# Optimization experiments

Hardware: AMD Instinct MI355X
Metric: run time of the kernel (lower is better)

## Reference

```python
import jax, jax.numpy as jnp
import numpy as np

NUM_GRAPHS = 512
EPS_BN = 1e-5


def _bn(x, g, b):
    # BatchNorm1d in training mode: biased batch statistics over node dim
    m = x.mean(0)
    v = x.var(0)
    return g * (x - m) * jax.lax.rsqrt(v + EPS_BN) + b


def _gcn(x, W, b, src, dst):
    # GCNConv with self-loops and symmetric deg^-1/2 normalization
    n = x.shape[0]
    loop = jnp.arange(n, dtype=src.dtype)
    s = jnp.concatenate([src, loop])
    d = jnp.concatenate([dst, loop])
    h = x @ W  # [N, C_out]
    deg = jax.ops.segment_sum(jnp.ones(d.shape[0], dtype=h.dtype), d, num_segments=n)
    dinv = jax.lax.rsqrt(jnp.maximum(deg, 1.0))  # deg >= 1 due to self-loops
    norm = dinv[s] * dinv[d]  # [E+N]
    out = jax.ops.segment_sum(norm[:, None] * h[s], d, num_segments=n)
    return out + b


def setup_inputs() -> dict:
    key = jax.random.key(0)
    ks = jax.random.split(key, 16)
    N, E, F = 100000, 1600000, 6

    def lin(k, fi, fo):
        k1, k2 = jax.random.split(k)
        s = 1.0 / np.sqrt(fi)
        return (jax.random.uniform(k1, (fi, fo), minval=-s, maxval=s),
                jax.random.uniform(k2, (fo,), minval=-s, maxval=s))

    W1, b1 = lin(ks[0], F, 32)
    W2, b2 = lin(ks[1], 32, 64)
    W3, b3 = lin(ks[2], 64, 128)
    Wf1, bf1 = lin(ks[3], 128, 128)
    Wf2, bf2 = lin(ks[4], 128, 64)
    return {
        "x": jax.random.normal(ks[5], (N, F), dtype=jnp.float32),
        "edge_src": jax.random.randint(ks[6], (E,), 0, N, dtype=jnp.int32),
        "edge_dst": jax.random.randint(ks[7], (E,), 0, N, dtype=jnp.int32),
        "batch": jnp.sort(jax.random.randint(ks[8], (N,), 0, NUM_GRAPHS, dtype=jnp.int32)),
        "W1": W1, "b1": b1, "g1": jnp.ones(32), "be1": jnp.zeros(32),
        "W2": W2, "b2": b2, "g2": jnp.ones(64), "be2": jnp.zeros(64),
        "W3": W3, "b3": b3, "g3": jnp.ones(128), "be3": jnp.zeros(128),
        "Wf1": Wf1, "bf1": bf1, "g4": jnp.ones(128), "be4": jnp.zeros(128),
        "Wf2": Wf2, "bf2": bf2,
    }


def reference(x, edge_src, edge_dst, batch,
              W1, b1, g1, be1, W2, b2, g2, be2, W3, b3, g3, be3,
              Wf1, bf1, g4, be4, Wf2, bf2):
    h = jax.nn.relu(_bn(_gcn(x, W1, b1, edge_src, edge_dst), g1, be1))
    h = jax.nn.relu(_bn(_gcn(h, W2, b2, edge_src, edge_dst), g2, be2))
    h = jax.nn.relu(_bn(_gcn(h, W3, b3, edge_src, edge_dst), g3, be3))
    p = jax.ops.segment_max(h, batch, num_segments=NUM_GRAPHS)  # [G, 128]
    p = jax.nn.relu(_bn(p @ Wf1 + bf1, g4, be4))  # dropout = identity (eval)
    p = p @ Wf2 + bf2
    return p / jnp.maximum(jnp.linalg.norm(p, axis=1, keepdims=True), 1e-12)
```

## Files before the change

### kernel.cpp

```cpp
#include <hip/hip_runtime.h>
#include <hip/hip_bf16.h>

#define NG 512
#define EPS_BN 1e-5f

__device__ __forceinline__ float4 f4add(float4 a, float4 b) {
    a.x += b.x; a.y += b.y; a.z += b.z; a.w += b.w; return a;
}
__device__ __forceinline__ float4 f4fma(float s, float4 b, float4 a) {
    a.x = fmaf(s, b.x, a.x); a.y = fmaf(s, b.y, a.y);
    a.z = fmaf(s, b.z, a.z); a.w = fmaf(s, b.w, a.w); return a;
}
__device__ __forceinline__ float4 f4scale(float s, float4 a) {
    a.x *= s; a.y *= s; a.z *= s; a.w *= s; return a;
}
__device__ __forceinline__ float4 bnrelu4(float4 v, float4 sc, float4 sh) {
    float4 r;
    r.x = fmaxf(fmaf(sc.x, v.x, sh.x), 0.f);
    r.y = fmaxf(fmaf(sc.y, v.y, sh.y), 0.f);
    r.z = fmaxf(fmaf(sc.z, v.z, sh.z), 0.f);
    r.w = fmaxf(fmaf(sc.w, v.w, sh.w), 0.f);
    return r;
}
__device__ __forceinline__ void bnparam(float sm, float sq, float ga, float bt,
                                        float invN, float& sc, float& sh) {
    float m = sm * invN;
    float var = fmaf(-m, m, sq * invN);
    sc = ga * rsqrtf(var + EPS_BN);
    sh = fmaf(-m, sc, bt);
}


__global__ void k_count(const int* __restrict__ dst, int* __restrict__ cnt, int E) {
    int i = blockIdx.x * blockDim.x + threadIdx.x;
    if (i < E) atomicAdd(&cnt[dst[i]], 1);
}

__global__ void k_dinv(const int* __restrict__ cnt, float* __restrict__ dinv, int N) {
    int i = blockIdx.x * blockDim.x + threadIdx.x;
    if (i < N) dinv[i] = rsqrtf((float)cnt[i] + 1.0f);
}


#define SCAN_T 256
#define SCAN_I 4

__global__ void k_scan1(const int* __restrict__ in, int* __restrict__ out,
                        int* __restrict__ bsum, int N) {
    __shared__ int lds[SCAN_T];
    int t = threadIdx.x;
    int base = blockIdx.x * (SCAN_T * SCAN_I) + t * SCAN_I;
    int v[SCAN_I];
    int sum = 0;
#pragma unroll
    for (int i = 0; i < SCAN_I; ++i) {
        int idx = base + i;
        v[i] = (idx < N) ? in[idx] : 0;
        sum += v[i];
    }
    lds[t] = sum;
    __syncthreads();
    for (int o = 1; o < SCAN_T; o <<= 1) {
        int a = (t >= o) ? lds[t - o] : 0;
        __syncthreads();
        lds[t] += a;
        __syncthreads();
    }
    int run = lds[t] - sum;
#pragma unroll
    for (int i = 0; i < SCAN_I; ++i) {
        int idx = base + i;
        if (idx < N) out[idx] = run;
        run += v[i];
    }
    if (t == SCAN_T - 1) bsum[blockIdx.x] = lds[SCAN_T - 1];
}

__global__ void k_scan2(int* __restrict__ bs, int nb) {
    __shared__ int lds[SCAN_T];
    int t = threadIdx.x;
    int runbase = 0;
    for (int start = 0; start < nb; start += SCAN_T) {
        int idx = start + t;
        int v = (idx < nb) ? bs[idx] : 0;
        lds[t] = v;
        __syncthreads();
        for (int o = 1; o < SCAN_T; o <<= 1) {
            int a = (t >= o) ? lds[t - o] : 0;
            __syncthreads();
            lds[t] += a;
            __syncthreads();
        }
        if (idx < nb) bs[idx] = runbase + lds[t] - v;
        int tot = lds[SCAN_T - 1];
        __syncthreads();
        runbase += tot;
    }
}

__global__ void k_scan3(int* __restrict__ out, const int* __restrict__ bs, int N) {
    int add = bs[blockIdx.x];
    int base = blockIdx.x * (SCAN_T * SCAN_I) + threadIdx.x * SCAN_I;
#pragma unroll
    for (int i = 0; i < SCAN_I; ++i) {
        int idx = base + i;
        if (idx < N) out[idx] += add;
    }
}


__global__ void k_bucket(const int* __restrict__ src, const int* __restrict__ dst,
                         const float* __restrict__ dinv, const int* __restrict__ rowptr,
                         int* __restrict__ fill, int* __restrict__ esrc,
                         float* __restrict__ ewt, int E) {
    int e = blockIdx.x * blockDim.x + threadIdx.x;
    if (e >= E) return;
    int d = dst[e], s = src[e];
    int pos = rowptr[d] + atomicAdd(&fill[d], 1);
    esrc[pos] = s;
    ewt[pos] = dinv[s];
}


template <int COUT>
__global__ __launch_bounds__(256) void k_layer1(
    const int* __restrict__ rowptr, const int* __restrict__ cnt,
    const int* __restrict__ esrc, const float* __restrict__ ewt,
    const float* __restrict__ dinv, const float* __restrict__ x,
    const float* __restrict__ W, float* __restrict__ hout,
    float* __restrict__ sums, float* __restrict__ sumsq, int N) {
    constexpr int NPB = 256;
    constexpr int CG = COUT / 4;
    constexpr int RPB = 256 / CG;
    __shared__ float4 inT4[NPB * 6 / 4];
    float* inT = (float*)inT4;
    __shared__ float4 wT[6 * CG];
    __shared__ float4 red[256];
    int t = threadIdx.x;
    const float4* W4 = (const float4*)W;
    for (int i = t; i < 6 * CG; i += 256) wT[i] = W4[i];
    int base = blockIdx.x * NPB;
    int n = base + t;
    if (n < N) {
        const float2* x2 = (const float2*)x;
        int beg = rowptr[n], end = beg + cnt[n];
        float di = dinv[n];
        size_t b3 = (size_t)n * 3;
        float2 p0 = x2[b3], p1 = x2[b3 + 1], p2 = x2[b3 + 2];
        float a0 = di * p0.x, a1 = di * p0.y, a2 = di * p1.x;
        float a3 = di * p1.y, a4 = di * p2.x, a5 = di * p2.y;
        for (int e = beg; e < end; ++e) {
            int s = esrc[e];
            float w = ewt[e];
            size_t s3 = (size_t)s * 3;
            float2 q0 = x2[s3], q1 = x2[s3 + 1], q2 = x2[s3 + 2];
            a0 = fmaf(w, q0.x, a0); a1 = fmaf(w, q0.y, a1);
            a2 = fmaf(w, q1.x, a2); a3 = fmaf(w, q1.y, a3);
            a4 = fmaf(w, q2.x, a4); a5 = fmaf(w, q2.y, a5);
        }
        int o = t * 6;
        inT[o + 0] = di * a0; inT[o + 1] = di * a1; inT[o + 2] = di * a2;
        inT[o + 3] = di * a3; inT[o + 4] = di * a4; inT[o + 5] = di * a5;
    }
    __syncthreads();
    int gi = t % CG, r0 = t / CG, c0 = gi * 4;
    int nrows = min(NPB, N - base);
    float4 s = {0, 0, 0, 0}, s2 = {0, 0, 0, 0};
    for (int r = r0; r < nrows; r += RPB) {
        const float* row = inT + r * 6;
        float4 acc = {0, 0, 0, 0};
#pragma unroll
        for (int k = 0; k < 6; ++k) acc = f4fma(row[k], wT[k * CG + gi], acc);
        reinterpret_cast<float4*>(hout + (size_t)(base + r) * COUT)[gi] = acc;
        s = f4add(s, acc);
        s2.x = fmaf(acc.x, acc.x, s2.x);
        s2.y = fmaf(acc.y, acc.y, s2.y);
        s2.z = fmaf(acc.z, acc.z, s2.z);
        s2.w = fmaf(acc.w, acc.w, s2.w);
    }
    red[t] = s;
    for (int hh = RPB / 2; hh > 0; hh >>= 1) {
        __syncthreads();
        if (r0 < hh) red[t] = f4add(red[t], red[t + hh * CG]);
    }
    if (r0 == 0) {
        float4 a = red[t];
        atomicAdd(&sums[c0 + 0], a.x); atomicAdd(&sums[c0 + 1], a.y);
        atomicAdd(&sums[c0 + 2], a.z); atomicAdd(&sums[c0 + 3], a.w);
    }
    __syncthreads();
    red[t] = s2;
    for (int hh = RPB / 2; hh > 0; hh >>= 1) {
        __syncthreads();
        if (r0 < hh) red[t] = f4add(red[t], red[t + hh * CG]);
    }
    if (r0 == 0) {
        float4 b = red[t];
        atomicAdd(&sumsq[c0 + 0], b.x); atomicAdd(&sumsq[c0 + 1], b.y);
        atomicAdd(&sumsq[c0 + 2], b.z); atomicAdd(&sumsq[c0 + 3], b.w);
    }
}


template <int CIN, int COUT, int NPB>
__global__ __launch_bounds__(256, 5) void k_layer(
    const int* __restrict__ rowptr, const int* __restrict__ cnt,
    const int* __restrict__ esrc, const float* __restrict__ ewt,
    const float* __restrict__ dinv, const float* __restrict__ hin,
    const float* __restrict__ sums_in, const float* __restrict__ sumsq_in,
    const float* __restrict__ gam, const float* __restrict__ bet,
    const float* __restrict__ W, float* __restrict__ hout,
    float* __restrict__ sums_out, float* __restrict__ sumsq_out,
    int N, float invN) {
    constexpr int TPN = CIN / 4;
    constexpr int PAD = TPN + 1;
    constexpr int ITER1 = NPB * TPN / 256;
    constexpr int NPI = 256 / TPN;
    constexpr int CG = COUT / 4;
    constexpr int RPB = 256 / CG;
    __shared__ float4 inT4[NPB * PAD];
    __shared__ float4 red[256];
    int t = threadIdx.x;
    const float4* W4 = (const float4*)W;
    int base = blockIdx.x * NPB;
    {
        int c4 = t % TPN;
        float4 sm = reinterpret_cast<const float4*>(sums_in)[c4];
        float4 sq = reinterpret_cast<const float4*>(sumsq_in)[c4];
        float4 ga = reinterpret_cast<const float4*>(gam)[c4];
        float4 bt = reinterpret_cast<const float4*>(bet)[c4];
        float4 sc, sh;
        bnparam(sm.x, sq.x, ga.x, bt.x, invN, sc.x, sh.x);
        bnparam(sm.y, sq.y, ga.y, bt.y, invN, sc.y, sh.y);
        bnparam(sm.z, sq.z, ga.z, bt.z, invN, sc.z, sh.z);
        bnparam(sm.w, sq.w, ga.w, bt.w, invN, sc.w, sh.w);
        const float4* h4 = reinterpret_cast<const float4*>(hin);
#pragma unroll
        for (int it = 0; it < ITER1; ++it) {
            int nl = it * NPI + t / TPN;
            int n = base + nl;
            if (n < N) {
                int beg = rowptr[n], end = beg + cnt[n];
                float di = dinv[n];
                float4 acc = f4scale(di, bnrelu4(h4[(size_t)n * TPN + c4], sc, sh));
                int e = beg;
                for (; e + 3 < end; e += 4) {
                    int s0 = esrc[e], s1 = esrc[e + 1], s2_ = esrc[e + 2], s3_ = esrc[e + 3];
                    float w0 = ewt[e], w1 = ewt[e + 1], w2 = ewt[e + 2], w3 = ewt[e + 3];
                    float4 v0 = h4[(size_t)s0 * TPN + c4];
                    float4 v1 = h4[(size_t)s1 * TPN + c4];
                    float4 v2 = h4[(size_t)s2_ * TPN + c4];
                    float4 v3 = h4[(size_t)s3_ * TPN + c4];
                    acc = f4fma(w0, bnrelu4(v0, sc, sh), acc);
                    acc = f4fma(w1, bnrelu4(v1, sc, sh), acc);
                    acc = f4fma(w2, bnrelu4(v2, sc, sh), acc);
                    acc = f4fma(w3, bnrelu4(v3, sc, sh), acc);
                }
                for (; e + 1 < end; e += 2) {
                    int s0 = esrc[e], s1 = esrc[e + 1];
                    float w0 = ewt[e], w1 = ewt[e + 1];
                    float4 v0 = h4[(size_t)s0 * TPN + c4];
                    float4 v1 = h4[(size_t)s1 * TPN + c4];
                    acc = f4fma(w0, bnrelu4(v0, sc, sh), acc);
                    acc = f4fma(w1, bnrelu4(v1, sc, sh), acc);
                }
                if (e < end)
                    acc = f4fma(ewt[e], bnrelu4(h4[(size_t)esrc[e] * TPN + c4], sc, sh), acc);
                inT4[nl * PAD + c4] = f4scale(di, acc);
            }
        }
    }
    __syncthreads();
    int gi = t % CG, r0 = t / CG, c0 = gi * 4;
    int nrows = min(NPB, N - base);
    float4 s = {0, 0, 0, 0}, s2 = {0, 0, 0, 0};
    for (int r = r0; r < nrows; r += RPB) {
        const float* row = (const float*)(inT4 + r * PAD);
        float4 acc = {0, 0, 0, 0};
#pragma unroll 8
        for (int k = 0; k < CIN; ++k) acc = f4fma(row[k], W4[k * CG + gi], acc);
        reinterpret_cast<float4*>(hout + (size_t)(base + r) * COUT)[gi] = acc;
        s = f4add(s, acc);
        s2.x = fmaf(acc.x, acc.x, s2.x);
        s2.y = fmaf(acc.y, acc.y, s2.y);
        s2.z = fmaf(acc.z, acc.z, s2.z);
        s2.w = fmaf(acc.w, acc.w, s2.w);
    }
    red[t] = s;
    for (int hh = RPB / 2; hh > 0; hh >>= 1) {
        __syncthreads();
        if (r0 < hh) red[t] = f4add(red[t], red[t + hh * CG]);
    }
    if (r0 == 0) {
        float4 a = red[t];
        atomicAdd(&sums_out[c0 + 0], a.x); atomicAdd(&sums_out[c0 + 1], a.y);
        atomicAdd(&sums_out[c0 + 2], a.z); atomicAdd(&sums_out[c0 + 3], a.w);
    }
    __syncthreads();
    red[t] = s2;
    for (int hh = RPB / 2; hh > 0; hh >>= 1) {
        __syncthreads();
        if (r0 < hh) red[t] = f4add(red[t], red[t + hh * CG]);
    }
    if (r0 == 0) {
        float4 b = red[t];
        atomicAdd(&sumsq_out[c0 + 0], b.x); atomicAdd(&sumsq_out[c0 + 1], b.y);
        atomicAdd(&sumsq_out[c0 + 2], b.z); atomicAdd(&sumsq_out[c0 + 3], b.w);
    }
}


template <int CIN, int COUT, int ROWS>
__global__ __launch_bounds__(256) void k_mm_stats(
    const float* __restrict__ in, const float* __restrict__ W,
    float* __restrict__ out, float* __restrict__ sums,
    float* __restrict__ sumsq, int N) {
    constexpr int CG = COUT / 4;
    constexpr int RPB = 256 / CG;
    __shared__ float4 inT4[ROWS * CIN / 4];
    float* inT = (float*)inT4;
    __shared__ float4 wT[CIN * CG];
    __shared__ float4 red[256];
    int t = threadIdx.x;
    const float4* W4 = reinterpret_cast<const float4*>(W);
    for (int i = t; i < CIN * CG; i += 256) wT[i] = W4[i];
    int base = blockIdx.x * ROWS;
    int nrows = min(ROWS, N - base);
    {
        const float4* in4 = reinterpret_cast<const float4*>(in + (size_t)base * CIN);
        int tot = nrows * (CIN / 4);
        for (int i = t; i < tot; i += 256) inT4[i] = in4[i];
    }
    __syncthreads();
    int gi = t % CG, r0 = t / CG, c0 = gi * 4;
    float4 s = {0, 0, 0, 0}, s2 = {0, 0, 0, 0};
    for (int r = r0; r < nrows; r += RPB) {
        const float* row = inT + r * CIN;
        float4 acc = {0, 0, 0, 0};
#pragma unroll
        for (int k = 0; k < CIN; ++k) acc = f4fma(row[k], wT[k * CG + gi], acc);
        reinterpret_cast<float4*>(out + (size_t)(base + r) * COUT)[gi] = acc;
        s = f4add(s, acc);
        s2.x = fmaf(acc.x, acc.x, s2.x);
        s2.y = fmaf(acc.y, acc.y, s2.y);
        s2.z = fmaf(acc.z, acc.z, s2.z);
        s2.w = fmaf(acc.w, acc.w, s2.w);
    }
    red[t] = s;
    for (int hh = RPB / 2; hh > 0; hh >>= 1) {
        __syncthreads();
        if (r0 < hh) red[t] = f4add(red[t], red[t + hh * CG]);
    }
    if (r0 == 0) {
        float4 a = red[t];
        atomicAdd(&sums[c0 + 0], a.x); atomicAdd(&sums[c0 + 1], a.y);
        atomicAdd(&sums[c0 + 2], a.z); atomicAdd(&sums[c0 + 3], a.w);
    }
    __syncthreads();
    red[t] = s2;
    for (int hh = RPB / 2; hh > 0; hh >>= 1) {
        __syncthreads();
        if (r0 < hh) red[t] = f4add(red[t], red[t + hh * CG]);
    }
    if (r0 == 0) {
        float4 b = red[t];
        atomicAdd(&sumsq[c0 + 0], b.x); atomicAdd(&sumsq[c0 + 1], b.y);
        atomicAdd(&sumsq[c0 + 2], b.z); atomicAdd(&sumsq[c0 + 3], b.w);
    }
}


__global__ void k_segmax_bn(const float* __restrict__ h, const int* __restrict__ batch,
                            const float* __restrict__ sums, const float* __restrict__ sumsq,
                            const float* __restrict__ gam, const float* __restrict__ bet,
                            float* __restrict__ pool, int N, float invN) {
    int t = threadIdx.x;
    int c = t & 127;
    int sub = t >> 7;
    int base = blockIdx.x * 64 + sub * 32;
    if (base >= N) return;
    float sc, sh;
    bnparam(sums[c], sumsq[c], gam[c], bet[c], invN, sc, sh);
    int cur = batch[base];
    float mx = fmaxf(fmaf(sc, h[(size_t)base * 128 + c], sh), 0.f);
    int lim = min(32, N - base);
    for (int i = 1; i < lim; ++i) {
        int n = base + i;
        int b = batch[n];
        float v = fmaxf(fmaf(sc, h[(size_t)n * 128 + c], sh), 0.f);
        if (b != cur) {
            atomicMax(reinterpret_cast<int*>(pool) + (cur << 7) + c, __float_as_int(mx));
            cur = b; mx = v;
        } else {
            mx = fmaxf(mx, v);
        }
    }
    atomicMax(reinterpret_cast<int*>(pool) + (cur << 7) + c, __float_as_int(mx));
}


__global__ void k_head(const float* __restrict__ Z, const float* __restrict__ sums,
                       const float* __restrict__ sumsq, const float* __restrict__ gam,
                       const float* __restrict__ bet, const float* __restrict__ Wf2,
                       const float* __restrict__ bf2, float* __restrict__ out) {
    int g = blockIdx.x, c = threadIdx.x;
    __shared__ float row[128];
    const float invG = 1.0f / (float)NG;
    for (int j = c; j < 128; j += 64) {
        float sc, sh;
        bnparam(sums[j], sumsq[j], gam[j], bet[j], invG, sc, sh);
        row[j] = fmaxf(fmaf(sc, Z[(g << 7) + j], sh), 0.f);
    }
    __syncthreads();
    float acc = bf2[c];
#pragma unroll
    for (int k = 0; k < 128; ++k) acc = fmaf(row[k], Wf2[k * 64 + c], acc);
    float ss = acc * acc;
#pragma unroll
    for (int off = 32; off; off >>= 1) ss += __shfl_xor(ss, off);
    out[(g << 6) + c] = acc / fmaxf(sqrtf(ss), 1e-12f);
}


extern "C" void kernel_launch(void* const* d_in, const int* in_sizes, int n_in,
                              void* d_out, int out_size, void* d_ws, size_t ws_size,
                              hipStream_t stream) {
    const float* x    = (const float*)d_in[0];
    const int*   src  = (const int*)d_in[1];
    const int*   dst  = (const int*)d_in[2];
    const int*   batch= (const int*)d_in[3];
    const float* W1   = (const float*)d_in[4];
    const float* g1   = (const float*)d_in[6];
    const float* be1  = (const float*)d_in[7];
    const float* W2   = (const float*)d_in[8];
    const float* g2   = (const float*)d_in[10];
    const float* be2  = (const float*)d_in[11];
    const float* W3   = (const float*)d_in[12];
    const float* g3   = (const float*)d_in[14];
    const float* be3  = (const float*)d_in[15];
    const float* Wf1  = (const float*)d_in[16];
    const float* g4   = (const float*)d_in[18];
    const float* be4  = (const float*)d_in[19];
    const float* Wf2  = (const float*)d_in[20];
    const float* bf2  = (const float*)d_in[21];
    float* out = (float*)d_out;

    const int N = in_sizes[0] / 6;
    const int E = in_sizes[1];
    const int nScanBlocks = (N + SCAN_T * SCAN_I - 1) / (SCAN_T * SCAN_I);

    char* ws = (char*)d_ws;
    size_t off = 0;
    auto carve = [&](size_t bytes) {
        void* p = ws + off;
        off += (bytes + 255) & ~(size_t)255;
        return p;
    };
    int*   cnt    = (int*)carve((size_t)N * 4);
    float* dinv   = (float*)carve((size_t)N * 4);
    int*   rowptr = (int*)carve((size_t)N * 4);
    int*   fill   = (int*)carve((size_t)N * 4);
    int*   bsum   = (int*)carve((size_t)4096 * 4);
    int*   esrc   = (int*)carve((size_t)E * 4);
    float* ewt    = (float*)carve((size_t)E * 4);
    float* H1     = (float*)carve((size_t)N * 32 * 4);
    float* H2     = (float*)carve((size_t)N * 64 * 4);
    float* H3     = (float*)carve((size_t)N * 128 * 4);
    float* stats  = (float*)carve(704 * 4);
    float* pool   = (float*)carve((size_t)NG * 128 * 4);
    float* Z      = (float*)carve((size_t)NG * 128 * 4);
    float* s1 = stats;
    float* s2 = stats + 64;
    float* s3 = stats + 192;
    float* s4 = stats + 448;

    const float invN = 1.0f / (float)N;

    hipMemsetAsync(cnt, 0, (size_t)N * 4, stream);
    hipMemsetAsync(fill, 0, (size_t)N * 4, stream);
    hipMemsetAsync(stats, 0, 704 * 4, stream);
    hipMemsetAsync(pool, 0, (size_t)NG * 128 * 4, stream);
    k_count<<<(E + 255) / 256, 256, 0, stream>>>(dst, cnt, E);
    k_dinv<<<(N + 255) / 256, 256, 0, stream>>>(cnt, dinv, N);
    k_scan1<<<nScanBlocks, SCAN_T, 0, stream>>>(cnt, rowptr, bsum, N);
    k_scan2<<<1, SCAN_T, 0, stream>>>(bsum, nScanBlocks);
    k_scan3<<<nScanBlocks, SCAN_T, 0, stream>>>(rowptr, bsum, N);
    k_bucket<<<(E + 255) / 256, 256, 0, stream>>>(src, dst, dinv, rowptr, fill, esrc, ewt, E);

    k_layer1<32><<<(N + 255) / 256, 256, 0, stream>>>(
        rowptr, cnt, esrc, ewt, dinv, x, W1, H1, s1, s1 + 32, N);

    k_layer<32, 64, 64><<<(N + 63) / 64, 256, 0, stream>>>(
        rowptr, cnt, esrc, ewt, dinv, H1, s1, s1 + 32, g1, be1, W2, H2,
        s2, s2 + 64, N, invN);

    k_layer<64, 128, 64><<<(N + 63) / 64, 256, 0, stream>>>(
        rowptr, cnt, esrc, ewt, dinv, H2, s2, s2 + 64, g2, be2, W3, H3,
        s3, s3 + 128, N, invN);

    k_segmax_bn<<<(N + 63) / 64, 256, 0, stream>>>(H3, batch, s3, s3 + 128, g3, be3, pool, N, invN);

    k_mm_stats<128, 128, 64><<<(NG + 63) / 64, 256, 0, stream>>>(pool, Wf1, Z, s4, s4 + 128, NG);
    k_head<<<NG, 64, 0, stream>>>(Z, s4, s4 + 128, g4, be4, Wf2, bf2, out);
}
```

Baseline: 815.1 us.

## Split each node's edge list across lanes and pack edge src/weight pairs

Packs each CSR edge's source index and weight into one int2 array, so the aggregation loops do one 8-byte load per edge instead of two separate loads. Layer 1 and the hidden-layer kernels now split each node's neighbour list across 4 lanes and combine the partial sums with xor shuffles. This raises memory-level parallelism in the gather loops and spreads work more evenly across nodes of different degree. Blocks now process 32 nodes (NPB 32) with a higher occupancy launch bound, at the cost of more blocks and extra shuffle traffic.

```diff
diff --git a/kernel.cpp b/kernel.cpp
--- a/kernel.cpp
+++ b/kernel.cpp
@@ -28,6 +28,13 @@
     float var = fmaf(-m, m, sq * invN);
     sc = ga * rsqrtf(var + EPS_BN);
     sh = fmaf(-m, sc, bt);
+}
+__device__ __forceinline__ float4 f4shflxor_add(float4 a, int m) {
+    a.x += __shfl_xor(a.x, m);
+    a.y += __shfl_xor(a.y, m);
+    a.z += __shfl_xor(a.z, m);
+    a.w += __shfl_xor(a.w, m);
+    return a;
 }
 
 
@@ -111,56 +118,87 @@
 
 __global__ void k_bucket(const int* __restrict__ src, const int* __restrict__ dst,
                          const float* __restrict__ dinv, const int* __restrict__ rowptr,
-                         int* __restrict__ fill, int* __restrict__ esrc,
-                         float* __restrict__ ewt, int E) {
+                         int* __restrict__ fill, int2* __restrict__ e2, int E) {
     int e = blockIdx.x * blockDim.x + threadIdx.x;
     if (e >= E) return;
     int d = dst[e], s = src[e];
     int pos = rowptr[d] + atomicAdd(&fill[d], 1);
-    esrc[pos] = s;
-    ewt[pos] = dinv[s];
+    e2[pos] = make_int2(s, __float_as_int(dinv[s]));
 }
 
 
 template <int COUT>
 __global__ __launch_bounds__(256) void k_layer1(
     const int* __restrict__ rowptr, const int* __restrict__ cnt,
-    const int* __restrict__ esrc, const float* __restrict__ ewt,
-    const float* __restrict__ dinv, const float* __restrict__ x,
-    const float* __restrict__ W, float* __restrict__ hout,
-    float* __restrict__ sums, float* __restrict__ sumsq, int N) {
+    const int2* __restrict__ e2, const float* __restrict__ dinv,
+    const float* __restrict__ x, const float* __restrict__ W,
+    float* __restrict__ hout, float* __restrict__ sums,
+    float* __restrict__ sumsq, int N) {
     constexpr int NPB = 256;
     constexpr int CG = COUT / 4;
     constexpr int RPB = 256 / CG;
-    __shared__ float4 inT4[NPB * 6 / 4];
-    float* inT = (float*)inT4;
+    __shared__ float inT[NPB * 6];
     __shared__ float4 wT[6 * CG];
     __shared__ float4 red[256];
     int t = threadIdx.x;
     const float4* W4 = (const float4*)W;
     for (int i = t; i < 6 * CG; i += 256) wT[i] = W4[i];
     int base = blockIdx.x * NPB;
-    int n = base + t;
-    if (n < N) {
+    {
         const float2* x2 = (const float2*)x;
-        int beg = rowptr[n], end = beg + cnt[n];
-        float di = dinv[n];
-        size_t b3 = (size_t)n * 3;
-        float2 p0 = x2[b3], p1 = x2[b3 + 1], p2 = x2[b3 + 2];
-        float a0 = di * p0.x, a1 = di * p0.y, a2 = di * p1.x;
-        float a3 = di * p1.y, a4 = di * p2.x, a5 = di * p2.y;
-        for (int e = beg; e < end; ++e) {
-            int s = esrc[e];
-            float w = ewt[e];
-            size_t s3 = (size_t)s * 3;
-            float2 q0 = x2[s3], q1 = x2[s3 + 1], q2 = x2[s3 + 2];
-            a0 = fmaf(w, q0.x, a0); a1 = fmaf(w, q0.y, a1);
-            a2 = fmaf(w, q1.x, a2); a3 = fmaf(w, q1.y, a3);
-            a4 = fmaf(w, q2.x, a4); a5 = fmaf(w, q2.y, a5);
+        int ew = t & 3;
+        int nl0 = t >> 2;
+#pragma unroll 1
+        for (int it = 0; it < 4; ++it) {
+            int nl = it * 64 + nl0;
+            int n = base + nl;
+            float a0 = 0, a1 = 0, a2 = 0, a3 = 0, a4 = 0, a5 = 0;
+            float di = 0.f;
+            if (n < N) {
+                di = dinv[n];
+                int beg = rowptr[n], end = beg + cnt[n];
+                if (ew == 0) {
+                    size_t b3 = (size_t)n * 3;
+                    float2 p0 = x2[b3], p1 = x2[b3 + 1], p2 = x2[b3 + 2];
+                    a0 = di * p0.x; a1 = di * p0.y; a2 = di * p1.x;
+                    a3 = di * p1.y; a4 = di * p2.x; a5 = di * p2.y;
+                }
+                int e = beg + ew;
+                for (; e + 4 < end; e += 8) {
+                    int2 pa = e2[e], pb = e2[e + 4];
+                    size_t sa = (size_t)pa.x * 3, sb = (size_t)pb.x * 3;
+                    float2 qa0 = x2[sa], qa1 = x2[sa + 1], qa2 = x2[sa + 2];
+                    float2 qb0 = x2[sb], qb1 = x2[sb + 1], qb2 = x2[sb + 2];
+                    float wa = __int_as_float(pa.y), wb = __int_as_float(pb.y);
+                    a0 = fmaf(wa, qa0.x, a0); a1 = fmaf(wa, qa0.y, a1);
+                    a2 = fmaf(wa, qa1.x, a2); a3 = fmaf(wa, qa1.y, a3);
+                    a4 = fmaf(wa, qa2.x, a4); a5 = fmaf(wa, qa2.y, a5);
+                    a0 = fmaf(wb, qb0.x, a0); a1 = fmaf(wb, qb0.y, a1);
+                    a2 = fmaf(wb, qb1.x, a2); a3 = fmaf(wb, qb1.y, a3);
+                    a4 = fmaf(wb, qb2.x, a4); a5 = fmaf(wb, qb2.y, a5);
+                }
+                if (e < end) {
+                    int2 pa = e2[e];
+                    size_t sa = (size_t)pa.x * 3;
+                    float2 qa0 = x2[sa], qa1 = x2[sa + 1], qa2 = x2[sa + 2];
+                    float wa = __int_as_float(pa.y);
+                    a0 = fmaf(wa, qa0.x, a0); a1 = fmaf(wa, qa0.y, a1);
+                    a2 = fmaf(wa, qa1.x, a2); a3 = fmaf(wa, qa1.y, a3);
+                    a4 = fmaf(wa, qa2.x, a4); a5 = fmaf(wa, qa2.y, a5);
+                }
+            }
+#pragma unroll
+            for (int m = 1; m < 4; m <<= 1) {
+                a0 += __shfl_xor(a0, m); a1 += __shfl_xor(a1, m);
+                a2 += __shfl_xor(a2, m); a3 += __shfl_xor(a3, m);
+                a4 += __shfl_xor(a4, m); a5 += __shfl_xor(a5, m);
+            }
+            if (ew == 0 && n < N) {
+                int o = nl * 6;
+                inT[o + 0] = di * a0; inT[o + 1] = di * a1; inT[o + 2] = di * a2;
+                inT[o + 3] = di * a3; inT[o + 4] = di * a4; inT[o + 5] = di * a5;
+            }
         }
-        int o = t * 6;
-        inT[o + 0] = di * a0; inT[o + 1] = di * a1; inT[o + 2] = di * a2;
-        inT[o + 3] = di * a3; inT[o + 4] = di * a4; inT[o + 5] = di * a5;
     }
     __syncthreads();
     int gi = t % CG, r0 = t / CG, c0 = gi * 4;
@@ -202,20 +240,21 @@
 }
 
 
-template <int CIN, int COUT, int NPB>
-__global__ __launch_bounds__(256, 5) void k_layer(
+template <int CIN, int COUT, int NPB, int EW>
+__global__ __launch_bounds__(256, 8) void k_layer(
     const int* __restrict__ rowptr, const int* __restrict__ cnt,
-    const int* __restrict__ esrc, const float* __restrict__ ewt,
-    const float* __restrict__ dinv, const float* __restrict__ hin,
+    const int2* __restrict__ e2, const float* __restrict__ dinv,
+    const float* __restrict__ hin,
     const float* __restrict__ sums_in, const float* __restrict__ sumsq_in,
     const float* __restrict__ gam, const float* __restrict__ bet,
     const float* __restrict__ W, float* __restrict__ hout,
     float* __restrict__ sums_out, float* __restrict__ sumsq_out,
     int N, float invN) {
     constexpr int TPN = CIN / 4;
+    constexpr int LPN = TPN * EW;
+    constexpr int NPI = 256 / LPN;
+    constexpr int ITER1 = NPB / NPI;
     constexpr int PAD = TPN + 1;
-    constexpr int ITER1 = NPB * TPN / 256;
-    constexpr int NPI = 256 / TPN;
     constexpr int CG = COUT / 4;
     constexpr int RPB = 256 / CG;
     __shared__ float4 inT4[NPB * PAD];
@@ -225,6 +264,8 @@
     int base = blockIdx.x * NPB;
     {
         int c4 = t % TPN;
+        int ew = (t % LPN) / TPN;
+        int nl0 = t / LPN;
         float4 sm = reinterpret_cast<const float4*>(sums_in)[c4];
         float4 sq = reinterpret_cast<const float4*>(sumsq_in)[c4];
         float4 ga = reinterpret_cast<const float4*>(gam)[c4];
@@ -235,39 +276,34 @@
         bnparam(sm.z, sq.z, ga.z, bt.z, invN, sc.z, sh.z);
         bnparam(sm.w, sq.w, ga.w, bt.w, invN, sc.w, sh.w);
         const float4* h4 = reinterpret_cast<const float4*>(hin);
-#pragma unroll
+#pragma unroll 1
         for (int it = 0; it < ITER1; ++it) {
-            int nl = it * NPI + t / TPN;
+            int nl = it * NPI + nl0;
             int n = base + nl;
+            float4 acc = {0, 0, 0, 0};
+            float di = 0.f;
             if (n < N) {
+                di = dinv[n];
                 int beg = rowptr[n], end = beg + cnt[n];
-                float di = dinv[n];
-                float4 acc = f4scale(di, bnrelu4(h4[(size_t)n * TPN + c4], sc, sh));
-                int e = beg;
-                for (; e + 3 < end; e += 4) {
-                    int s0 = esrc[e], s1 = esrc[e + 1], s2_ = esrc[e + 2], s3_ = esrc[e + 3];
-                    float w0 = ewt[e], w1 = ewt[e + 1], w2 = ewt[e + 2], w3 = ewt[e + 3];
-                    float4 v0 = h4[(size_t)s0 * TPN + c4];
-                    float4 v1 = h4[(size_t)s1 * TPN + c4];
-                    float4 v2 = h4[(size_t)s2_ * TPN + c4];
-                    float4 v3 = h4[(size_t)s3_ * TPN + c4];
-                    acc = f4fma(w0, bnrelu4(v0, sc, sh), acc);
-                    acc = f4fma(w1, bnrelu4(v1, sc, sh), acc);
-                    acc = f4fma(w2, bnrelu4(v2, sc, sh), acc);
-                    acc = f4fma(w3, bnrelu4(v3, sc, sh), acc);
+                if (ew == 0)
+                    acc = f4scale(di, bnrelu4(h4[(size_t)n * TPN + c4], sc, sh));
+                int e = beg + ew;
+                for (; e + EW < end; e += 2 * EW) {
+                    int2 pa = e2[e], pb = e2[e + EW];
+                    float4 va = h4[(size_t)pa.x * TPN + c4];
+                    float4 vb = h4[(size_t)pb.x * TPN + c4];
+                    acc = f4fma(__int_as_float(pa.y), bnrelu4(va, sc, sh), acc);
+                    acc = f4fma(__int_as_float(pb.y), bnrelu4(vb, sc, sh), acc);
                 }
-                for (; e + 1 < end; e += 2) {
-                    int s0 = esrc[e], s1 = esrc[e + 1];
-                    float w0 = ewt[e], w1 = ewt[e + 1];
-                    float4 v0 = h4[(size_t)s0 * TPN + c4];
-                    float4 v1 = h4[(size_t)s1 * TPN + c4];
-                    acc = f4fma(w0, bnrelu4(v0, sc, sh), acc);
-                    acc = f4fma(w1, bnrelu4(v1, sc, sh), acc);
+                if (e < end) {
+                    int2 pa = e2[e];
+                    acc = f4fma(__int_as_float(pa.y),
+                                bnrelu4(h4[(size_t)pa.x * TPN + c4], sc, sh), acc);
                 }
-                if (e < end)
-                    acc = f4fma(ewt[e], bnrelu4(h4[(size_t)esrc[e] * TPN + c4], sc, sh), acc);
-                inT4[nl * PAD + c4] = f4scale(di, acc);
             }
+#pragma unroll
+            for (int m = TPN; m < LPN; m <<= 1) acc = f4shflxor_add(acc, m);
+            if (ew == 0 && n < N) inT4[nl * PAD + c4] = f4scale(di, acc);
         }
     }
     __syncthreads();
@@ -461,8 +497,7 @@
     int*   rowptr = (int*)carve((size_t)N * 4);
     int*   fill   = (int*)carve((size_t)N * 4);
     int*   bsum   = (int*)carve((size_t)4096 * 4);
-    int*   esrc   = (int*)carve((size_t)E * 4);
-    float* ewt    = (float*)carve((size_t)E * 4);
+    int2*  e2     = (int2*)carve((size_t)E * 8);
     float* H1     = (float*)carve((size_t)N * 32 * 4);
     float* H2     = (float*)carve((size_t)N * 64 * 4);
     float* H3     = (float*)carve((size_t)N * 128 * 4);
@@ -485,17 +520,17 @@
     k_scan1<<<nScanBlocks, SCAN_T, 0, stream>>>(cnt, rowptr, bsum, N);
     k_scan2<<<1, SCAN_T, 0, stream>>>(bsum, nScanBlocks);
     k_scan3<<<nScanBlocks, SCAN_T, 0, stream>>>(rowptr, bsum, N);
-    k_bucket<<<(E + 255) / 256, 256, 0, stream>>>(src, dst, dinv, rowptr, fill, esrc, ewt, E);
+    k_bucket<<<(E + 255) / 256, 256, 0, stream>>>(src, dst, dinv, rowptr, fill, e2, E);
 
     k_layer1<32><<<(N + 255) / 256, 256, 0, stream>>>(
-        rowptr, cnt, esrc, ewt, dinv, x, W1, H1, s1, s1 + 32, N);
-
-    k_layer<32, 64, 64><<<(N + 63) / 64, 256, 0, stream>>>(
-        rowptr, cnt, esrc, ewt, dinv, H1, s1, s1 + 32, g1, be1, W2, H2,
+        rowptr, cnt, e2, dinv, x, W1, H1, s1, s1 + 32, N);
+
+    k_layer<32, 64, 32, 4><<<(N + 31) / 32, 256, 0, stream>>>(
+        rowptr, cnt, e2, dinv, H1, s1, s1 + 32, g1, be1, W2, H2,
         s2, s2 + 64, N, invN);
 
-    k_layer<64, 128, 64><<<(N + 63) / 64, 256, 0, stream>>>(
-        rowptr, cnt, esrc, ewt, dinv, H2, s2, s2 + 64, g2, be2, W3, H3,
+    k_layer<64, 128, 32, 4><<<(N + 31) / 32, 256, 0, stream>>>(
+        rowptr, cnt, e2, dinv, H2, s2, s2 + 64, g2, be2, W3, H3,
         s3, s3 + 128, N, invN);
 
     k_segmax_bn<<<(N + 63) / 64, 256, 0, stream>>>(H3, batch, s3, s3 + 128, g3, be3, pool, N, invN);
```

Result: slower. 1.131 ms (+38.7%).
